# Kernel optimization log

Measured on AMD Instinct MI355X. Metric: run time of the kernel, lower is better.

The kernel has to match this reference:

```python
import jax, jax.numpy as jnp
import numpy as np

N_NODES = 20000
N_EDGES = 320000
NUM_RELS = 16
IN_FEAT = 256
OUT_FEAT = 256


def setup_inputs() -> dict:
    key = jax.random.key(0)
    k_h, k_w, k_n, k_s, k_d, k_r = jax.random.split(key, 6)
    h = jax.random.normal(k_h, (N_NODES, IN_FEAT), dtype=jnp.float32)
    weight = jax.random.normal(k_w, (NUM_RELS, IN_FEAT, OUT_FEAT), dtype=jnp.float32)
    norm = jax.random.uniform(k_n, (N_EDGES, 1), dtype=jnp.float32)
    src = jax.random.randint(k_s, (N_EDGES,), 0, N_NODES, dtype=jnp.int32)
    dst = jax.random.randint(k_d, (N_EDGES,), 0, N_NODES, dtype=jnp.int32)
    rel_type = jax.random.randint(k_r, (N_EDGES,), 0, NUM_RELS, dtype=jnp.int32)
    return {"h": h, "weight": weight, "norm": norm, "src": src, "dst": dst, "rel_type": rel_type}


def reference(h, weight, norm, src, dst, rel_type):
    # Transform every node feature by every relation weight once ([R, N, O]),
    # instead of gathering a full [E, in, out] weight tensor per edge.
    transformed = jnp.einsum('ni,rio->rno', h, weight)
    # Per-edge message: h[src] @ W[rel] scaled by edge norm -> [E, O]
    msg = transformed[rel_type, src] * norm
    # Scatter-sum messages into destination nodes (DGL mailbox sum reduce).
    out = jax.ops.segment_sum(msg, dst, num_segments=h.shape[0])
    # bias=None, activation=None in this configuration, so apply_func is identity.
    return out
```

## Files before the change

kernel.cpp:

```cpp
#include <hip/hip_runtime.h>
#include <stdint.h>

#define N_NODES_C 20000
#define N_EDGES_C 320000
#define NUM_RELS_C 16
#define FEAT_C 256
#define CAP_LOG2 6
#define GEMM_BLOCKS 5024
#define WS_FAST_BYTES 186497152ULL

typedef __bf16 bf16_t;
typedef __bf16 bf16x8 __attribute__((ext_vector_type(8)));
typedef __bf16 bf16x4 __attribute__((ext_vector_type(4)));
typedef float f32x4 __attribute__((ext_vector_type(4)));

__device__ __forceinline__ void async_load16(const void* g, void* l) {
  __builtin_amdgcn_global_load_lds(
      (__attribute__((address_space(1))) void*)const_cast<void*>(g),
      (__attribute__((address_space(3))) void*)l, 16, 0, 0);
}

__global__ void prep_fast_kernel(const float* __restrict__ h, bf16_t* __restrict__ hB,
                                 const float* __restrict__ W, bf16_t* __restrict__ Wt,
                                 int* __restrict__ cnt) {
  int b = blockIdx.x;
  int t = threadIdx.x;
  if (b < 5000) {
    int i = (b * 256 + t) * 4;
    float4 v = *(const float4*)(h + i);
    bf16x4 o = { (bf16_t)v.x, (bf16_t)v.y, (bf16_t)v.z, (bf16_t)v.w };
    *(bf16x4*)(hB + i) = o;
  } else if (b < 5256) {
    __shared__ bf16_t lds[64][66];
    int b2 = b - 5000;
    int r  = b2 >> 4;
    int i0 = ((b2 >> 2) & 3) << 6;
    int o0 = (b2 & 3) << 6;
    int tx = t & 15;
    int ty = t >> 4;
#pragma unroll
    for (int pass = 0; pass < 4; ++pass) {
      int il = ty + pass * 16;
      float4 v = *(const float4*)(W + (r << 16) + ((i0 + il) << 8) + o0 + tx * 4);
      lds[tx * 4 + 0][il] = (bf16_t)v.x;
      lds[tx * 4 + 1][il] = (bf16_t)v.y;
      lds[tx * 4 + 2][il] = (bf16_t)v.z;
      lds[tx * 4 + 3][il] = (bf16_t)v.w;
    }
    __syncthreads();
#pragma unroll
    for (int pass = 0; pass < 4; ++pass) {
      int ol = ty + pass * 16;
      bf16x4 pk = { lds[ol][tx * 4 + 0], lds[ol][tx * 4 + 1],
                    lds[ol][tx * 4 + 2], lds[ol][tx * 4 + 3] };
      *(bf16x4*)(Wt + (r << 16) + ((o0 + ol) << 8) + i0 + tx * 4) = pk;
    }
  } else {
    int idx = (b - 5256) * 256 + t;
    if (idx < N_NODES_C) cnt[idx] = 0;
  }
}

__global__ void prep_kernel(const float* __restrict__ h, bf16_t* __restrict__ hB,
                            const float* __restrict__ W, bf16_t* __restrict__ Wt,
                            const int* __restrict__ dst, int* __restrict__ dcur) {
  int b = blockIdx.x;
  int t = threadIdx.x;
  if (b < 5000) {
    int i = (b * 256 + t) * 4;
    float4 v = *(const float4*)(h + i);
    bf16x4 o = { (bf16_t)v.x, (bf16_t)v.y, (bf16_t)v.z, (bf16_t)v.w };
    *(bf16x4*)(hB + i) = o;
  } else if (b < 9096) {
    int g = (b - 5000) * 256 + t;
    int i = g & 255;
    int o = (g >> 8) & 255;
    int r = g >> 16;
    Wt[(r << 16) + (o << 8) + i] = (bf16_t)W[(r << 16) + (i << 8) + o];
  } else {
    int e = (b - 9096) * 256 + t;
    if (e < N_EDGES_C) atomicAdd(&dcur[dst[e]], 1);
  }
}

__global__ void scan_dst_kernel(int* __restrict__ dcur, int* __restrict__ dstart) {
  __shared__ unsigned short cnt[20224];
  __shared__ int wsum[4];
  const int CH = 79;
  int t = threadIdx.x;
  int base = t * CH;
  int sum = 0;
  for (int i = 0; i < CH; ++i) {
    int idx = base + i;
    int c = (idx < N_NODES_C) ? dcur[idx] : 0;
    cnt[idx] = (unsigned short)c;
    sum += c;
  }
  int v = sum;
#pragma unroll
  for (int off = 1; off < 64; off <<= 1) {
    int u = __shfl_up(v, off);
    if ((t & 63) >= off) v += u;
  }
  if ((t & 63) == 63) wsum[t >> 6] = v;
  __syncthreads();
  int add = 0;
  for (int w = 0; w < (t >> 6); ++w) add += wsum[w];
  int run = v - sum + add;
  for (int i = 0; i < CH; ++i) {
    int idx = base + i;
    if (idx < N_NODES_C) {
      int c = cnt[idx];
      dstart[idx] = run;
      dcur[idx] = run;
      run += c;
    }
  }
  if (t == 0) dstart[N_NODES_C] = N_EDGES_C;
}

__global__ void bucket_dst_kernel(const int* __restrict__ dst, const int* __restrict__ src,
                                  const int* __restrict__ rel, const float* __restrict__ norm,
                                  int* __restrict__ dcur, int2* __restrict__ bkt) {
  int e = blockIdx.x * blockDim.x + threadIdx.x;
  if (e < N_EDGES_C) {
    int pos = atomicAdd(&dcur[dst[e]], 1);
    int2 pk;
    pk.x = src[e] | (rel[e] << 16);
    pk.y = __float_as_int(norm[e]);
    bkt[pos] = pk;
  }
}

__global__ __launch_bounds__(256) void gemm_bucket_kernel(
    const bf16_t* __restrict__ hB, const bf16_t* __restrict__ Wt,
    bf16_t* __restrict__ Tb,
    const int* __restrict__ dst, const int* __restrict__ src,
    const int* __restrict__ rel, const float* __restrict__ norm,
    int* __restrict__ cnt, int2* __restrict__ bkt) {
  int bx = blockIdx.x;
  int tid = threadIdx.x;

  if (bx >= GEMM_BLOCKS) {
    int e = (bx - GEMM_BLOCKS) * 256 + tid;
    if (e < N_EDGES_C) {
      int d = dst[e];
      int pos = (d << CAP_LOG2) + atomicAdd(&cnt[d], 1);
      int2 pk;
      pk.x = src[e] | (rel[e] << 16);
      pk.y = __float_as_int(norm[e]);
      bkt[pos] = pk;
    }
    return;
  }

  int sub = bx & 31;
  int m0 = (bx >> 5) << 7;
  int r  = sub >> 1;
  int n0 = (sub & 1) << 7;

  __shared__ bf16_t Asm[3 * 128 * 32];
  __shared__ bf16_t Bsm[3 * 128 * 32];

  int lrow = tid >> 2;
  int pch = tid & 3;
  int rA0 = lrow, rA1 = lrow + 64;
  int lc0 = pch ^ ((rA0 >> 1) & 3);
  int lc1 = pch ^ ((rA1 >> 1) & 3);
  int gr0 = m0 + rA0; if (gr0 > N_NODES_C - 1) gr0 = N_NODES_C - 1;
  int gr1 = m0 + rA1; if (gr1 > N_NODES_C - 1) gr1 = N_NODES_C - 1;
  const char* gA0 = (const char*)(hB + (size_t)gr0 * FEAT_C) + lc0 * 16;
  const char* gA1 = (const char*)(hB + (size_t)gr1 * FEAT_C) + lc1 * 16;
  const char* gB0 = (const char*)(Wt + ((size_t)r * 256 + n0 + rA0) * FEAT_C) + lc0 * 16;
  const char* gB1 = (const char*)(Wt + ((size_t)r * 256 + n0 + rA1) * FEAT_C) + lc1 * 16;

  int wave = tid >> 6;
  int lane = tid & 63;
  int lq = lane >> 4;
  int lr = lane & 15;
  int wm = (wave >> 1) * 64;
  int wn = (wave & 1) * 64;
  int pc8 = (lq ^ ((lr >> 1) & 3)) * 8;

  f32x4 acc[4][4] = {};

#define STAGE(buf, t)                                             \
  do {                                                            \
    int kb_ = (t) * 64;                                           \
    char* aB_ = (char*)Asm + (buf) * 8192 + wave * 1024;          \
    char* bB_ = (char*)Bsm + (buf) * 8192 + wave * 1024;          \
    async_load16(gA0 + kb_, aB_);                                 \
    async_load16(gA1 + kb_, aB_ + 4096);                          \
    async_load16(gB0 + kb_, bB_);                                 \
    async_load16(gB1 + kb_, bB_ + 4096);                          \
  } while (0)

  STAGE(0, 0);
  STAGE(1, 1);

#pragma unroll
  for (int kk = 0; kk < 8; ++kk) {
    if (kk < 7) asm volatile("s_waitcnt vmcnt(4)" ::: "memory");
    else        asm volatile("s_waitcnt vmcnt(0)" ::: "memory");
    __builtin_amdgcn_s_barrier();
    __builtin_amdgcn_sched_barrier(0);
    const bf16_t* Ac = Asm + (kk % 3) * 4096;
    const bf16_t* Bc = Bsm + (kk % 3) * 4096;
    bf16x8 af[4], bfr[4];
#pragma unroll
    for (int mt = 0; mt < 4; ++mt) {
      int row = wm + mt * 16 + lr;
      af[mt] = *(const bf16x8*)&Ac[row * 32 + pc8];
    }
#pragma unroll
    for (int nt2 = 0; nt2 < 4; ++nt2) {
      int row = wn + nt2 * 16 + lr;
      bfr[nt2] = *(const bf16x8*)&Bc[row * 32 + pc8];
    }
    if (kk < 6) STAGE((kk + 2) % 3, kk + 2);
#pragma unroll
    for (int mt = 0; mt < 4; ++mt)
#pragma unroll
      for (int nt2 = 0; nt2 < 4; ++nt2)
        acc[mt][nt2] = __builtin_amdgcn_mfma_f32_16x16x32_bf16(af[mt], bfr[nt2], acc[mt][nt2], 0, 0, 0);
  }
#undef STAGE

#pragma unroll
  for (int mt = 0; mt < 4; ++mt) {
#pragma unroll
    for (int a = 0; a < 2; ++a) {
      int rg0 = a * 2, rg1 = rg0 + 1;
      union { bf16x4 v; long long u; } q0, q1;
      q0.v = (bf16x4){ (bf16_t)acc[mt][0][rg0], (bf16_t)acc[mt][1][rg0],
                       (bf16_t)acc[mt][2][rg0], (bf16_t)acc[mt][3][rg0] };
      q1.v = (bf16x4){ (bf16_t)acc[mt][0][rg1], (bf16_t)acc[mt][1][rg1],
                       (bf16_t)acc[mt][2][rg1], (bf16_t)acc[mt][3][rg1] };
      int odd = lr & 1;
      long long send = odd ? q0.u : q1.u;
      long long got = __shfl_xor(send, 1);
      union { bf16x8 v; long long u[2]; } w;
      w.u[0] = odd ? got : q0.u;
      w.u[1] = odd ? q1.u : got;
      int rg = rg0 + odd;
      int row = m0 + wm + mt * 16 + lq * 4 + rg;
      if (row < N_NODES_C) {
        int pos = n0 + wn + ((lr >> 1) << 3);
        *(bf16x8*)(Tb + (((size_t)r * N_NODES_C + row) << 8) + pos) = w.v;
      }
    }
  }
}

template <int MODE>
__global__ __launch_bounds__(256) void aggregate_kernel(
    const bf16_t* __restrict__ Tb, const int* __restrict__ meta,
    const int2* __restrict__ bkt, float* __restrict__ out) {
  int tid = threadIdx.x;
  int d = blockIdx.x * 4 + (tid >> 6);
  int lane = tid & 63;
  int p0, p1;
  if (MODE == 0) { p0 = meta[d]; p1 = meta[d + 1]; }
  else           { p0 = d << CAP_LOG2; p1 = p0 + meta[d]; }
  int boff = lane << 3;
  float a0 = 0.f, a1 = 0.f, a2 = 0.f, a3 = 0.f;
  int p = p0;
  for (; p + 8 <= p1; p += 8) {
    int2 m[8];
#pragma unroll
    for (int q = 0; q < 8; ++q) m[q] = bkt[p + q];
    bf16x4 v[8];
#pragma unroll
    for (int q = 0; q < 8; ++q)
      v[q] = *(const bf16x4*)((const char*)(Tb + (((size_t)(m[q].x >> 16) * N_NODES_C + (m[q].x & 0xFFFF)) << 8)) + boff);
#pragma unroll
    for (int q = 0; q < 8; ++q) {
      float nq = __int_as_float(m[q].y);
      a0 += (float)v[q][0] * nq;
      a1 += (float)v[q][1] * nq;
      a2 += (float)v[q][2] * nq;
      a3 += (float)v[q][3] * nq;
    }
  }
  if (p + 4 <= p1) {
    int2 m[4];
#pragma unroll
    for (int q = 0; q < 4; ++q) m[q] = bkt[p + q];
    bf16x4 v[4];
#pragma unroll
    for (int q = 0; q < 4; ++q)
      v[q] = *(const bf16x4*)((const char*)(Tb + (((size_t)(m[q].x >> 16) * N_NODES_C + (m[q].x & 0xFFFF)) << 8)) + boff);
#pragma unroll
    for (int q = 0; q < 4; ++q) {
      float nq = __int_as_float(m[q].y);
      a0 += (float)v[q][0] * nq;
      a1 += (float)v[q][1] * nq;
      a2 += (float)v[q][2] * nq;
      a3 += (float)v[q][3] * nq;
    }
    p += 4;
  }
  for (; p < p1; ++p) {
    int2 m0 = bkt[p];
    bf16x4 v0 = *(const bf16x4*)((const char*)(Tb + (((size_t)(m0.x >> 16) * N_NODES_C + (m0.x & 0xFFFF)) << 8)) + boff);
    float n0 = __int_as_float(m0.y);
    a0 += (float)v0[0] * n0;
    a1 += (float)v0[1] * n0;
    a2 += (float)v0[2] * n0;
    a3 += (float)v0[3] * n0;
  }
  float* o = out + (size_t)d * FEAT_C + ((lane << 2) & 192) + (lane & 15);
  o[0]  = a0;
  o[16] = a1;
  o[32] = a2;
  o[48] = a3;
}

extern "C" void kernel_launch(void* const* d_in, const int* in_sizes, int n_in,
                              void* d_out, int out_size, void* d_ws, size_t ws_size,
                              hipStream_t stream) {
  const float* h    = (const float*)d_in[0];
  const float* W    = (const float*)d_in[1];
  const float* norm = (const float*)d_in[2];
  const int*   src  = (const int*)d_in[3];
  const int*   dst  = (const int*)d_in[4];
  const int*   rel  = (const int*)d_in[5];
  float* out = (float*)d_out;

  char* ws = (char*)d_ws;
  bf16_t* hB   = (bf16_t*)ws;
  bf16_t* Wt   = (bf16_t*)(ws + 10240000);
  bf16_t* Tb   = (bf16_t*)(ws + 12337152);

  if (ws_size >= WS_FAST_BYTES) {
    int* cnt  = (int*)(ws + 176177152);
    int2* bkt = (int2*)(ws + 176257152);
    prep_fast_kernel<<<5335, 256, 0, stream>>>(h, hB, W, Wt, cnt);
    gemm_bucket_kernel<<<GEMM_BLOCKS + 1250, 256, 0, stream>>>(
        hB, Wt, Tb, dst, src, rel, norm, cnt, bkt);
    aggregate_kernel<1><<<5000, 256, 0, stream>>>(Tb, cnt, bkt, out);
  } else {
    int* dstart  = (int*)(ws + 176177152);
    int* dcur    = (int*)(ws + 176257168);
    int2* bkt    = (int2*)(ws + 176337168);
    hipMemsetAsync(dcur, 0, N_NODES_C * sizeof(int), stream);
    prep_kernel<<<10346, 256, 0, stream>>>(h, hB, W, Wt, dst, dcur);
    scan_dst_kernel<<<1, 256, 0, stream>>>(dcur, dstart);
    bucket_dst_kernel<<<1250, 256, 0, stream>>>(dst, src, rel, norm, dcur, bkt);
    gemm_bucket_kernel<<<GEMM_BLOCKS, 256, 0, stream>>>(
        hB, Wt, Tb, nullptr, nullptr, nullptr, nullptr, nullptr, nullptr);
    aggregate_kernel<0><<<5000, 256, 0, stream>>>(Tb, dstart, bkt, out);
  }
}
```

Measured before the change: 182.7 us.

## Split GEMM by relation halves and overlap first-half aggregation with second GEMM

Moves the edge bucketing from the GEMM kernel into the prep kernel and zeroes the counters with a memset. The per-relation GEMM is split into two launches covering relations 0-7 and 8-15. The second launch also carries aggregation blocks that sum messages from relations 0-7, so that gather work overlaps with GEMM compute. A final kernel adds the contributions from relations 8-15 with a read-modify-write on the output. The cost is extra launches, scanning the edge bucket list twice, and an extra read and write of the output.

New measurement: 221.6 us. 1.21x slower.

```diff
diff --git a/kernel.cpp b/kernel.cpp
--- a/kernel.cpp
+++ b/kernel.cpp
@@ -6,7 +6,7 @@
 #define NUM_RELS_C 16
 #define FEAT_C 256
 #define CAP_LOG2 6
-#define GEMM_BLOCKS 5024
+#define GEMM_HALF_BLOCKS 2512
 #define WS_FAST_BYTES 186497152ULL
 
 typedef __bf16 bf16_t;
@@ -20,9 +20,62 @@
       (__attribute__((address_space(3))) void*)l, 16, 0, 0);
 }
 
+template <int PART, int ACCUM>
+__device__ __forceinline__ void agg_body(int blk, int tid,
+                                         const bf16_t* __restrict__ Tb,
+                                         const int* __restrict__ cnt,
+                                         const int2* __restrict__ bkt,
+                                         float* __restrict__ out) {
+  int d = blk * 4 + (tid >> 6);
+  int lane = tid & 63;
+  int p0 = d << CAP_LOG2;
+  int p1 = p0 + cnt[d];
+  int boff = lane << 3;
+  float a0 = 0.f, a1 = 0.f, a2 = 0.f, a3 = 0.f;
+  int p = p0;
+  for (; p + 8 <= p1; p += 8) {
+    int2 m[8];
+#pragma unroll
+    for (int q = 0; q < 8; ++q) m[q] = bkt[p + q];
+    bf16x4 v[8];
+#pragma unroll
+    for (int q = 0; q < 8; ++q)
+      if (PART < 0 || ((m[q].x >> 19) & 1) == PART)
+        v[q] = *(const bf16x4*)((const char*)(Tb + (((size_t)(m[q].x >> 16) * N_NODES_C + (m[q].x & 0xFFFF)) << 8)) + boff);
+#pragma unroll
+    for (int q = 0; q < 8; ++q)
+      if (PART < 0 || ((m[q].x >> 19) & 1) == PART) {
+        float nq = __int_as_float(m[q].y);
+        a0 += (float)v[q][0] * nq;
+        a1 += (float)v[q][1] * nq;
+        a2 += (float)v[q][2] * nq;
+        a3 += (float)v[q][3] * nq;
+      }
+  }
+  for (; p < p1; ++p) {
+    int2 mm = bkt[p];
+    if (PART < 0 || ((mm.x >> 19) & 1) == PART) {
+      bf16x4 v0 = *(const bf16x4*)((const char*)(Tb + (((size_t)(mm.x >> 16) * N_NODES_C + (mm.x & 0xFFFF)) << 8)) + boff);
+      float n0 = __int_as_float(mm.y);
+      a0 += (float)v0[0] * n0;
+      a1 += (float)v0[1] * n0;
+      a2 += (float)v0[2] * n0;
+      a3 += (float)v0[3] * n0;
+    }
+  }
+  float* o = out + (size_t)d * FEAT_C + ((lane << 2) & 192) + (lane & 15);
+  if (ACCUM) {
+    o[0] += a0; o[16] += a1; o[32] += a2; o[48] += a3;
+  } else {
+    o[0] = a0; o[16] = a1; o[32] = a2; o[48] = a3;
+  }
+}
+
 __global__ void prep_fast_kernel(const float* __restrict__ h, bf16_t* __restrict__ hB,
                                  const float* __restrict__ W, bf16_t* __restrict__ Wt,
-                                 int* __restrict__ cnt) {
+                                 const int* __restrict__ dst, const int* __restrict__ src,
+                                 const int* __restrict__ rel, const float* __restrict__ norm,
+                                 int* __restrict__ cnt, int2* __restrict__ bkt) {
   int b = blockIdx.x;
   int t = threadIdx.x;
   if (b < 5000) {
@@ -56,9 +109,133 @@
       *(bf16x4*)(Wt + (r << 16) + ((o0 + ol) << 8) + i0 + tx * 4) = pk;
     }
   } else {
-    int idx = (b - 5256) * 256 + t;
-    if (idx < N_NODES_C) cnt[idx] = 0;
-  }
+    int e = (b - 5256) * 256 + t;
+    if (e < N_EDGES_C) {
+      int d = dst[e];
+      int pos = (d << CAP_LOG2) + atomicAdd(&cnt[d], 1);
+      int2 pk;
+      pk.x = src[e] | (rel[e] << 16);
+      pk.y = __float_as_int(norm[e]);
+      bkt[pos] = pk;
+    }
+  }
+}
+
+template <int RBASE, bool TAIL>
+__global__ __launch_bounds__(256) void gemm_agg_kernel(
+    const bf16_t* __restrict__ hB, const bf16_t* __restrict__ Wt,
+    bf16_t* __restrict__ Tb, const int* __restrict__ cnt,
+    const int2* __restrict__ bkt, float* __restrict__ out) {
+  int bx = blockIdx.x;
+  int tid = threadIdx.x;
+
+  if (TAIL && bx >= GEMM_HALF_BLOCKS) {
+    agg_body<0, 0>(bx - GEMM_HALF_BLOCKS, tid, Tb, cnt, bkt, out);
+    return;
+  }
+
+  int sub = bx & 15;
+  int m0 = (bx >> 4) << 7;
+  int r  = RBASE + (sub >> 1);
+  int n0 = (sub & 1) << 7;
+
+  __shared__ bf16_t Asm[3 * 128 * 32];
+  __shared__ bf16_t Bsm[3 * 128 * 32];
+
+  int lrow = tid >> 2;
+  int pch = tid & 3;
+  int rA0 = lrow, rA1 = lrow + 64;
+  int lc0 = pch ^ ((rA0 >> 1) & 3);
+  int lc1 = pch ^ ((rA1 >> 1) & 3);
+  int gr0 = m0 + rA0; if (gr0 > N_NODES_C - 1) gr0 = N_NODES_C - 1;
+  int gr1 = m0 + rA1; if (gr1 > N_NODES_C - 1) gr1 = N_NODES_C - 1;
+  const char* gA0 = (const char*)(hB + (size_t)gr0 * FEAT_C) + lc0 * 16;
+  const char* gA1 = (const char*)(hB + (size_t)gr1 * FEAT_C) + lc1 * 16;
+  const char* gB0 = (const char*)(Wt + ((size_t)r * 256 + n0 + rA0) * FEAT_C) + lc0 * 16;
+  const char* gB1 = (const char*)(Wt + ((size_t)r * 256 + n0 + rA1) * FEAT_C) + lc1 * 16;
+
+  int wave = tid >> 6;
+  int lane = tid & 63;
+  int lq = lane >> 4;
+  int lr = lane & 15;
+  int wm = (wave >> 1) * 64;
+  int wn = (wave & 1) * 64;
+  int pc8 = (lq ^ ((lr >> 1) & 3)) * 8;
+
+  f32x4 acc[4][4] = {};
+
+#define STAGE(buf, t)                                             \
+  do {                                                            \
+    int kb_ = (t) * 64;                                           \
+    char* aB_ = (char*)Asm + (buf) * 8192 + wave * 1024;          \
+    char* bB_ = (char*)Bsm + (buf) * 8192 + wave * 1024;          \
+    async_load16(gA0 + kb_, aB_);                                 \
+    async_load16(gA1 + kb_, aB_ + 4096);                          \
+    async_load16(gB0 + kb_, bB_);                                 \
+    async_load16(gB1 + kb_, bB_ + 4096);                          \
+  } while (0)
+
+  STAGE(0, 0);
+  STAGE(1, 1);
+
+#pragma unroll
+  for (int kk = 0; kk < 8; ++kk) {
+    if (kk < 7) asm volatile("s_waitcnt vmcnt(4)" ::: "memory");
+    else        asm volatile("s_waitcnt vmcnt(0)" ::: "memory");
+    __builtin_amdgcn_s_barrier();
+    __builtin_amdgcn_sched_barrier(0);
+    const bf16_t* Ac = Asm + (kk % 3) * 4096;
+    const bf16_t* Bc = Bsm + (kk % 3) * 4096;
+    bf16x8 af[4], bfr[4];
+#pragma unroll
+    for (int mt = 0; mt < 4; ++mt) {
+      int row = wm + mt * 16 + lr;
+      af[mt] = *(const bf16x8*)&Ac[row * 32 + pc8];
+    }
+#pragma unroll
+    for (int nt2 = 0; nt2 < 4; ++nt2) {
+      int row = wn + nt2 * 16 + lr;
+      bfr[nt2] = *(const bf16x8*)&Bc[row * 32 + pc8];
+    }
+    if (kk < 6) STAGE((kk + 2) % 3, kk + 2);
+#pragma unroll
+    for (int mt = 0; mt < 4; ++mt)
+#pragma unroll
+      for (int nt2 = 0; nt2 < 4; ++nt2)
+        acc[mt][nt2] = __builtin_amdgcn_mfma_f32_16x16x32_bf16(af[mt], bfr[nt2], acc[mt][nt2], 0, 0, 0);
+  }
+#undef STAGE
+
+#pragma unroll
+  for (int mt = 0; mt < 4; ++mt) {
+#pragma unroll
+    for (int a = 0; a < 2; ++a) {
+      int rg0 = a * 2, rg1 = rg0 + 1;
+      union { bf16x4 v; long long u; } q0, q1;
+      q0.v = (bf16x4){ (bf16_t)acc[mt][0][rg0], (bf16_t)acc[mt][1][rg0],
+                       (bf16_t)acc[mt][2][rg0], (bf16_t)acc[mt][3][rg0] };
+      q1.v = (bf16x4){ (bf16_t)acc[mt][0][rg1], (bf16_t)acc[mt][1][rg1],
+                       (bf16_t)acc[mt][2][rg1], (bf16_t)acc[mt][3][rg1] };
+      int odd = lr & 1;
+      long long send = odd ? q0.u : q1.u;
+      long long got = __shfl_xor(send, 1);
+      union { bf16x8 v; long long u[2]; } w;
+      w.u[0] = odd ? got : q0.u;
+      w.u[1] = odd ? q1.u : got;
+      int rg = rg0 + odd;
+      int row = m0 + wm + mt * 16 + lq * 4 + rg;
+      if (row < N_NODES_C) {
+        int pos = n0 + wn + ((lr >> 1) << 3);
+        *(bf16x8*)(Tb + (((size_t)r * N_NODES_C + row) << 8) + pos) = w.v;
+      }
+    }
+  }
+}
+
+__global__ __launch_bounds__(256) void agg_partB_kernel(
+    const bf16_t* __restrict__ Tb, const int* __restrict__ cnt,
+    const int2* __restrict__ bkt, float* __restrict__ out) {
+  agg_body<1, 1>(blockIdx.x, threadIdx.x, Tb, cnt, bkt, out);
 }
 
 __global__ void prep_kernel(const float* __restrict__ h, bf16_t* __restrict__ hB,
@@ -132,136 +309,14 @@
   }
 }
 
-__global__ __launch_bounds__(256) void gemm_bucket_kernel(
-    const bf16_t* __restrict__ hB, const bf16_t* __restrict__ Wt,
-    bf16_t* __restrict__ Tb,
-    const int* __restrict__ dst, const int* __restrict__ src,
-    const int* __restrict__ rel, const float* __restrict__ norm,
-    int* __restrict__ cnt, int2* __restrict__ bkt) {
-  int bx = blockIdx.x;
-  int tid = threadIdx.x;
-
-  if (bx >= GEMM_BLOCKS) {
-    int e = (bx - GEMM_BLOCKS) * 256 + tid;
-    if (e < N_EDGES_C) {
-      int d = dst[e];
-      int pos = (d << CAP_LOG2) + atomicAdd(&cnt[d], 1);
-      int2 pk;
-      pk.x = src[e] | (rel[e] << 16);
-      pk.y = __float_as_int(norm[e]);
-      bkt[pos] = pk;
-    }
-    return;
-  }
-
-  int sub = bx & 31;
-  int m0 = (bx >> 5) << 7;
-  int r  = sub >> 1;
-  int n0 = (sub & 1) << 7;
-
-  __shared__ bf16_t Asm[3 * 128 * 32];
-  __shared__ bf16_t Bsm[3 * 128 * 32];
-
-  int lrow = tid >> 2;
-  int pch = tid & 3;
-  int rA0 = lrow, rA1 = lrow + 64;
-  int lc0 = pch ^ ((rA0 >> 1) & 3);
-  int lc1 = pch ^ ((rA1 >> 1) & 3);
-  int gr0 = m0 + rA0; if (gr0 > N_NODES_C - 1) gr0 = N_NODES_C - 1;
-  int gr1 = m0 + rA1; if (gr1 > N_NODES_C - 1) gr1 = N_NODES_C - 1;
-  const char* gA0 = (const char*)(hB + (size_t)gr0 * FEAT_C) + lc0 * 16;
-  const char* gA1 = (const char*)(hB + (size_t)gr1 * FEAT_C) + lc1 * 16;
-  const char* gB0 = (const char*)(Wt + ((size_t)r * 256 + n0 + rA0) * FEAT_C) + lc0 * 16;
-  const char* gB1 = (const char*)(Wt + ((size_t)r * 256 + n0 + rA1) * FEAT_C) + lc1 * 16;
-
-  int wave = tid >> 6;
-  int lane = tid & 63;
-  int lq = lane >> 4;
-  int lr = lane & 15;
-  int wm = (wave >> 1) * 64;
-  int wn = (wave & 1) * 64;
-  int pc8 = (lq ^ ((lr >> 1) & 3)) * 8;
-
-  f32x4 acc[4][4] = {};
-
-#define STAGE(buf, t)                                             \
-  do {                                                            \
-    int kb_ = (t) * 64;                                           \
-    char* aB_ = (char*)Asm + (buf) * 8192 + wave * 1024;          \
-    char* bB_ = (char*)Bsm + (buf) * 8192 + wave * 1024;          \
-    async_load16(gA0 + kb_, aB_);                                 \
-    async_load16(gA1 + kb_, aB_ + 4096);                          \
-    async_load16(gB0 + kb_, bB_);                                 \
-    async_load16(gB1 + kb_, bB_ + 4096);                          \
-  } while (0)
-
-  STAGE(0, 0);
-  STAGE(1, 1);
-
-#pragma unroll
-  for (int kk = 0; kk < 8; ++kk) {
-    if (kk < 7) asm volatile("s_waitcnt vmcnt(4)" ::: "memory");
-    else        asm volatile("s_waitcnt vmcnt(0)" ::: "memory");
-    __builtin_amdgcn_s_barrier();
-    __builtin_amdgcn_sched_barrier(0);
-    const bf16_t* Ac = Asm + (kk % 3) * 4096;
-    const bf16_t* Bc = Bsm + (kk % 3) * 4096;
-    bf16x8 af[4], bfr[4];
-#pragma unroll
-    for (int mt = 0; mt < 4; ++mt) {
-      int row = wm + mt * 16 + lr;
-      af[mt] = *(const bf16x8*)&Ac[row * 32 + pc8];
-    }
-#pragma unroll
-    for (int nt2 = 0; nt2 < 4; ++nt2) {
-      int row = wn + nt2 * 16 + lr;
-      bfr[nt2] = *(const bf16x8*)&Bc[row * 32 + pc8];
-    }
-    if (kk < 6) STAGE((kk + 2) % 3, kk + 2);
-#pragma unroll
-    for (int mt = 0; mt < 4; ++mt)
-#pragma unroll
-      for (int nt2 = 0; nt2 < 4; ++nt2)
-        acc[mt][nt2] = __builtin_amdgcn_mfma_f32_16x16x32_bf16(af[mt], bfr[nt2], acc[mt][nt2], 0, 0, 0);
-  }
-#undef STAGE
-
-#pragma unroll
-  for (int mt = 0; mt < 4; ++mt) {
-#pragma unroll
-    for (int a = 0; a < 2; ++a) {
-      int rg0 = a * 2, rg1 = rg0 + 1;
-      union { bf16x4 v; long long u; } q0, q1;
-      q0.v = (bf16x4){ (bf16_t)acc[mt][0][rg0], (bf16_t)acc[mt][1][rg0],
-                       (bf16_t)acc[mt][2][rg0], (bf16_t)acc[mt][3][rg0] };
-      q1.v = (bf16x4){ (bf16_t)acc[mt][0][rg1], (bf16_t)acc[mt][1][rg1],
-                       (bf16_t)acc[mt][2][rg1], (bf16_t)acc[mt][3][rg1] };
-      int odd = lr & 1;
-      long long send = odd ? q0.u : q1.u;
-      long long got = __shfl_xor(send, 1);
-      union { bf16x8 v; long long u[2]; } w;
-      w.u[0] = odd ? got : q0.u;
-      w.u[1] = odd ? q1.u : got;
-      int rg = rg0 + odd;
-      int row = m0 + wm + mt * 16 + lq * 4 + rg;
-      if (row < N_NODES_C) {
-        int pos = n0 + wn + ((lr >> 1) << 3);
-        *(bf16x8*)(Tb + (((size_t)r * N_NODES_C + row) << 8) + pos) = w.v;
-      }
-    }
-  }
-}
-
-template <int MODE>
-__global__ __launch_bounds__(256) void aggregate_kernel(
-    const bf16_t* __restrict__ Tb, const int* __restrict__ meta,
+__global__ __launch_bounds__(256) void aggregate_csr_kernel(
+    const bf16_t* __restrict__ Tb, const int* __restrict__ dstart,
     const int2* __restrict__ bkt, float* __restrict__ out) {
   int tid = threadIdx.x;
   int d = blockIdx.x * 4 + (tid >> 6);
   int lane = tid & 63;
-  int p0, p1;
-  if (MODE == 0) { p0 = meta[d]; p1 = meta[d + 1]; }
-  else           { p0 = d << CAP_LOG2; p1 = p0 + meta[d]; }
+  int p0 = dstart[d];
+  int p1 = dstart[d + 1];
   int boff = lane << 3;
   float a0 = 0.f, a1 = 0.f, a2 = 0.f, a3 = 0.f;
   int p = p0;
@@ -281,24 +336,6 @@
       a2 += (float)v[q][2] * nq;
       a3 += (float)v[q][3] * nq;
     }
-  }
-  if (p + 4 <= p1) {
-    int2 m[4];
-#pragma unroll
-    for (int q = 0; q < 4; ++q) m[q] = bkt[p + q];
-    bf16x4 v[4];
-#pragma unroll
-    for (int q = 0; q < 4; ++q)
-      v[q] = *(const bf16x4*)((const char*)(Tb + (((size_t)(m[q].x >> 16) * N_NODES_C + (m[q].x & 0xFFFF)) << 8)) + boff);
-#pragma unroll
-    for (int q = 0; q < 4; ++q) {
-      float nq = __int_as_float(m[q].y);
-      a0 += (float)v[q][0] * nq;
-      a1 += (float)v[q][1] * nq;
-      a2 += (float)v[q][2] * nq;
-      a3 += (float)v[q][3] * nq;
-    }
-    p += 4;
   }
   for (; p < p1; ++p) {
     int2 m0 = bkt[p];
@@ -335,10 +372,11 @@
   if (ws_size >= WS_FAST_BYTES) {
     int* cnt  = (int*)(ws + 176177152);
     int2* bkt = (int2*)(ws + 176257152);
-    prep_fast_kernel<<<5335, 256, 0, stream>>>(h, hB, W, Wt, cnt);
-    gemm_bucket_kernel<<<GEMM_BLOCKS + 1250, 256, 0, stream>>>(
-        hB, Wt, Tb, dst, src, rel, norm, cnt, bkt);
-    aggregate_kernel<1><<<5000, 256, 0, stream>>>(Tb, cnt, bkt, out);
+    hipMemsetAsync(cnt, 0, N_NODES_C * sizeof(int), stream);
+    prep_fast_kernel<<<6506, 256, 0, stream>>>(h, hB, W, Wt, dst, src, rel, norm, cnt, bkt);
+    gemm_agg_kernel<0, false><<<GEMM_HALF_BLOCKS, 256, 0, stream>>>(hB, Wt, Tb, cnt, bkt, out);
+    gemm_agg_kernel<8, true><<<GEMM_HALF_BLOCKS + 5000, 256, 0, stream>>>(hB, Wt, Tb, cnt, bkt, out);
+    agg_partB_kernel<<<5000, 256, 0, stream>>>(Tb, cnt, bkt, out);
   } else {
     int* dstart  = (int*)(ws + 176177152);
     int* dcur    = (int*)(ws + 176257168);
@@ -347,8 +385,8 @@
     prep_kernel<<<10346, 256, 0, stream>>>(h, hB, W, Wt, dst, dcur);
     scan_dst_kernel<<<1, 256, 0, stream>>>(dcur, dstart);
     bucket_dst_kernel<<<1250, 256, 0, stream>>>(dst, src, rel, norm, dcur, bkt);
-    gemm_bucket_kernel<<<GEMM_BLOCKS, 256, 0, stream>>>(
-        hB, Wt, Tb, nullptr, nullptr, nullptr, nullptr, nullptr, nullptr);
-    aggregate_kernel<0><<<5000, 256, 0, stream>>>(Tb, dstart, bkt, out);
-  }
-}
+    gemm_agg_kernel<0, false><<<GEMM_HALF_BLOCKS, 256, 0, stream>>>(hB, Wt, Tb, dstart, bkt, out);
+    gemm_agg_kernel<8, false><<<GEMM_HALF_BLOCKS, 256, 0, stream>>>(hB, Wt, Tb, dstart, bkt, out);
+    aggregate_csr_kernel<<<5000, 256, 0, stream>>>(Tb, dstart, bkt, out);
+  }
+}
```
